# Performance work log

Measured on AMD Instinct MI355X. Metric: run time of the kernel, lower is better.

## Reference

```python
import math
import jax, jax.numpy as jnp
import numpy as np

N_EMBD = 1024
N_HEAD = 16
HEAD_DIM = N_EMBD // N_HEAD


def setup_inputs() -> dict:
    key = jax.random.key(0)
    k1, k2, k3, k4, k5 = jax.random.split(key, 5)
    B, T, C = 1, 4096, N_EMBD
    s = 1.0 / math.sqrt(C)
    return {
        "x": jax.random.normal(k1, (B, T, C), dtype=jnp.float32),
        "w_qkv": jax.random.normal(k2, (C, 3 * C), dtype=jnp.float32) * s,
        "b_qkv": jnp.zeros((3 * C,), dtype=jnp.float32),
        "w_proj": jax.random.normal(k3, (C, C), dtype=jnp.float32) * s,
        "b_proj": jnp.zeros((C,), dtype=jnp.float32),
    }


def reference(x, w_qkv, b_qkv, w_proj, b_proj):
    B, T, C = x.shape
    qkv = x @ w_qkv + b_qkv                       # [B,T,3C]
    q, k, v = jnp.split(qkv, 3, axis=-1)
    # [B,T,C] -> [B,H,T,D]
    def heads(t):
        return t.reshape(B, T, N_HEAD, HEAD_DIM).transpose(0, 2, 1, 3)
    q, k, v = heads(q), heads(k), heads(v)
    scale = 1.0 / math.sqrt(HEAD_DIM)
    attn = jnp.einsum("bhqd,bhkd->bhqk", q, k) * scale
    causal = jnp.tril(jnp.ones((T, T), dtype=bool))
    attn = jnp.where(causal, attn, -jnp.inf)
    attn = jax.nn.softmax(attn, axis=-1)
    out = jnp.einsum("bhqk,bhkd->bhqd", attn, v)   # [B,H,T,D]
    out = out.transpose(0, 2, 1, 3).reshape(B, T, C)
    return out @ w_proj + b_proj
```

## Files before the change

kernel.cpp:

```cpp
#include <hip/hip_runtime.h>
#include <hip/hip_bf16.h>

#define TT 4096
#define CC 1024
#define NHEAD 16
#define DH 64
#define N3C 3072

typedef __attribute__((ext_vector_type(8))) short short8;
typedef __attribute__((ext_vector_type(4))) float floatx4;

#define QSCALE 0.18033688011112042f

__device__ __forceinline__ short f2bf(float f) {
    union { __hip_bfloat16 h; short s; } u;
    u.h = __float2bfloat16(f);
    return u.s;
}

__device__ __forceinline__ void gload_lds16(const void* g, void* l) {
    __builtin_amdgcn_global_load_lds(
        (const __attribute__((address_space(1))) unsigned int*)(unsigned long long)g,
        (__attribute__((address_space(3))) unsigned int*)(unsigned int)(unsigned long long)l,
        16, 0, 0);
}

__device__ __forceinline__ unsigned pk_trunc(float lo, float hi) {
    return __builtin_amdgcn_perm(__float_as_uint(hi), __float_as_uint(lo), 0x07060302u);
}

__device__ __forceinline__ void tr_body(const float* __restrict__ in, short* __restrict__ out,
                                        int K, int N, int bx, int by, int tid, float (*tile)[33]) {
    int nt = bx * 32, kt = by * 32;
    int tx = tid & 31, ty = tid >> 5;
#pragma unroll
    for (int i = 0; i < 32; i += 8)
        tile[ty + i][tx] = in[(size_t)(kt + ty + i) * N + nt + tx];
    __syncthreads();
#pragma unroll
    for (int i = 0; i < 32; i += 8)
        out[(size_t)(nt + ty + i) * K + kt + tx] = f2bf(tile[tx][ty + i]);
}

__global__ void k_prep(const float* __restrict__ x, short* __restrict__ xb,
                       const float* __restrict__ w_qkv, short* __restrict__ wqkvT,
                       const float* __restrict__ w_proj, short* __restrict__ wprojT) {
    __shared__ float tile[32][33];
    int id = blockIdx.x;
    int tid = threadIdx.x;
    if (id < 4096) {
        int i = (id * 256 + tid) * 4;
        float4 v = *(const float4*)&x[i];
        short4 r;
        r.x = f2bf(v.x); r.y = f2bf(v.y); r.z = f2bf(v.z); r.w = f2bf(v.w);
        *(short4*)&xb[i] = r;
    } else if (id < 4096 + 3072) {
        int r = id - 4096;
        tr_body(w_qkv, wqkvT, CC, N3C, r % 96, r / 96, tid, tile);
    } else {
        int r = id - 7168;
        tr_body(w_proj, wprojT, CC, CC, r & 31, r >> 5, tid, tile);
    }
}

__global__ __launch_bounds__(256) void k_gemm_qkv(const short* __restrict__ A,
                                                  const short* __restrict__ Bt,
                                                  const float* __restrict__ bias,
                                                  short* __restrict__ Q,
                                                  short* __restrict__ Kb,
                                                  short* __restrict__ Vtg) {
    const int m0 = blockIdx.y * 128;
    const int n0 = blockIdx.x * 128;
    __shared__ __attribute__((aligned(16))) short As[2][128 * 32];
    __shared__ __attribute__((aligned(16))) short Bs[2][128 * 32];
    const int tid = threadIdx.x;
    const int lane = tid & 63;
    const int w = tid >> 6;
    const int wm = w >> 1, wn = w & 1;
    const int quad = lane >> 4;
    const int l16 = lane & 15;

    const int r0 = tid >> 2, c0 = (tid & 3) * 8;
    const short* pA[2][2]; const short* pB[2][2];
    short* lA[2][2]; short* lB[2][2];
#pragma unroll
    for (int it = 0; it < 2; ++it)
#pragma unroll
        for (int hh = 0; hh < 2; ++hh) {
            pA[it][hh] = A + (size_t)(m0 + it * 64 + r0) * CC + hh * 32 + c0;
            pB[it][hh] = Bt + (size_t)(n0 + it * 64 + r0) * CC + hh * 32 + c0;
            lA[it][hh] = &As[hh][(it * 256 + w * 64) * 8];
            lB[it][hh] = &Bs[hh][(it * 256 + w * 64) * 8];
        }

    floatx4 acc[4][4] = {};
    for (int kb = 0; kb < CC; kb += 64) {
        __syncthreads();
#pragma unroll
        for (int it = 0; it < 2; ++it)
#pragma unroll
            for (int hh = 0; hh < 2; ++hh) {
                gload_lds16(pA[it][hh] + kb, lA[it][hh]);
                gload_lds16(pB[it][hh] + kb, lB[it][hh]);
            }
        __syncthreads();
#pragma unroll
        for (int kk = 0; kk < 2; ++kk) {
            short8 af[4], bf[4];
#pragma unroll
            for (int mi = 0; mi < 4; ++mi)
                af[mi] = *(const short8*)&As[kk][(wm * 64 + mi * 16 + l16) * 32 + quad * 8];
#pragma unroll
            for (int ni = 0; ni < 4; ++ni)
                bf[ni] = *(const short8*)&Bs[kk][(wn * 64 + ni * 16 + l16) * 32 + quad * 8];
#pragma unroll
            for (int mi = 0; mi < 4; ++mi)
#pragma unroll
                for (int ni = 0; ni < 4; ++ni)
                    acc[mi][ni] = __builtin_amdgcn_mfma_f32_16x16x32_bf16(af[mi], bf[ni], acc[mi][ni], 0, 0, 0);
        }
    }
#pragma unroll
    for (int mi = 0; mi < 4; ++mi) {
#pragma unroll
        for (int ni = 0; ni < 4; ++ni) {
            int gm = m0 + wm * 64 + mi * 16 + quad * 4;
            int gn = n0 + wn * 64 + ni * 16 + l16;
            int which = gn >> 10;
            int cc = gn & 1023;
            int h = cc >> 6, d = cc & 63;
            float bv = bias[gn];
            if (which == 0) {
#pragma unroll
                for (int r = 0; r < 4; ++r) {
                    float v = (acc[mi][ni][r] + bv) * QSCALE;
                    Q[((size_t)h * TT + (gm + r)) * DH + d] = f2bf(v);
                }
            } else if (which == 1) {
#pragma unroll
                for (int r = 0; r < 4; ++r) {
                    float v = acc[mi][ni][r] + bv;
                    Kb[((size_t)h * TT + (gm + r)) * DH + d] = f2bf(v);
                }
            } else {
                short4 vv;
                vv.x = f2bf(acc[mi][ni][0] + bv);
                vv.y = f2bf(acc[mi][ni][1] + bv);
                vv.z = f2bf(acc[mi][ni][2] + bv);
                vv.w = f2bf(acc[mi][ni][3] + bv);
                *(short4*)&Vtg[((size_t)h * DH + d) * TT + gm] = vv;
            }
        }
    }
}

__global__ __launch_bounds__(256) void k_attn(const short* __restrict__ Qh,
                                              const short* __restrict__ Kh,
                                              const short* __restrict__ VhT,
                                              short* __restrict__ Ob) {
    const int h = blockIdx.x;
    const int qi = 63 - blockIdx.y;
    const int tid = threadIdx.x, lane = tid & 63, w = tid >> 6;
    const int quad = lane >> 4, l16 = lane & 15;

    __shared__ __attribute__((aligned(16))) short Ps[2][64 * 136];
    __shared__ float wl[4][64];
    __shared__ float lsum[64];

    const short* Qp = Qh + (size_t)h * TT * DH;
    const short* Kp = Kh + (size_t)h * TT * DH;
    const short* Vp = VhT + (size_t)h * DH * TT;

    const int q0 = qi * 64;
    const int nk = (qi >> 1) + 1;

    short8 aq[4][2];
#pragma unroll
    for (int qg = 0; qg < 4; ++qg)
#pragma unroll
        for (int s = 0; s < 2; ++s)
            aq[qg][s] = *(const short8*)&Qp[(size_t)(q0 + qg * 16 + l16) * DH + s * 32 + quad * 8];

    floatx4 accO[4] = {};
    float l_part[4] = {0.f, 0.f, 0.f, 0.f};
    int buf = 0;

    for (int ki = 0; ki < nk; ++ki) {
        const int k0 = ki * 128;
        const bool masked = (ki == nk - 1);

        short8 kf[2][2];
#pragma unroll
        for (int mi = 0; mi < 2; ++mi)
#pragma unroll
            for (int s = 0; s < 2; ++s)
                kf[mi][s] = *(const short8*)&Kp[(size_t)(k0 + w * 32 + mi * 16 + l16) * DH + s * 32 + quad * 8];

        floatx4 accS[2][4] = {};
#pragma unroll
        for (int mi = 0; mi < 2; ++mi)
#pragma unroll
            for (int s = 0; s < 2; ++s)
#pragma unroll
                for (int qg = 0; qg < 4; ++qg)
                    accS[mi][qg] = __builtin_amdgcn_mfma_f32_16x16x32_bf16(kf[mi][s], aq[qg][s], accS[mi][qg], 0, 0, 0);

        short* Pb = &Ps[buf][0];
#pragma unroll
        for (int mi = 0; mi < 2; ++mi) {
            const int kbase = k0 + w * 32 + mi * 16 + quad * 4;
#pragma unroll
            for (int qg = 0; qg < 4; ++qg) {
                float p[4];
#pragma unroll
                for (int r = 0; r < 4; ++r) {
                    float e = __builtin_amdgcn_exp2f(accS[mi][qg][r]);
                    if (masked)
                        e = (kbase + r <= q0 + qg * 16 + l16) ? e : 0.f;
                    p[r] = e;
                    l_part[qg] += e;
                }
                uint2 pk;
                pk.x = pk_trunc(p[0], p[1]);
                pk.y = pk_trunc(p[2], p[3]);
                *(uint2*)&Pb[(qg * 16 + l16) * 136 + w * 32 + mi * 16 + quad * 4] = pk;
            }
        }

        short8 vf[4];
#pragma unroll
        for (int ks = 0; ks < 4; ++ks)
            vf[ks] = *(const short8*)&Vp[(size_t)(w * 16 + l16) * TT + k0 + ks * 32 + quad * 8];

        __syncthreads();

#pragma unroll
        for (int qg = 0; qg < 4; ++qg)
#pragma unroll
            for (int ks = 0; ks < 4; ++ks) {
                short8 ap = *(const short8*)&Pb[(qg * 16 + l16) * 136 + ks * 32 + quad * 8];
                accO[qg] = __builtin_amdgcn_mfma_f32_16x16x32_bf16(ap, vf[ks], accO[qg], 0, 0, 0);
            }
        buf ^= 1;
    }

#pragma unroll
    for (int qg = 0; qg < 4; ++qg) {
        float lr = l_part[qg];
        lr += __shfl_xor(lr, 16, 64);
        lr += __shfl_xor(lr, 32, 64);
        if (lane < 16) wl[w][qg * 16 + lane] = lr;
    }
    __syncthreads();
    if (tid < 64) lsum[tid] = wl[0][tid] + wl[1][tid] + wl[2][tid] + wl[3][tid];
    __syncthreads();

#pragma unroll
    for (int qg = 0; qg < 4; ++qg) {
#pragma unroll
        for (int r = 0; r < 4; ++r) {
            int q = qg * 16 + quad * 4 + r;
            float o = accO[qg][r] / lsum[q];
            Ob[(size_t)(q0 + q) * CC + h * DH + w * 16 + l16] = f2bf(o);
        }
    }
}

__global__ __launch_bounds__(256) void k_gemm_proj(const short* __restrict__ A,
                                                   const short* __restrict__ Bt,
                                                   const float* __restrict__ bias,
                                                   float* __restrict__ out) {
    const int m0 = blockIdx.y * 128;
    const int n0 = blockIdx.x * 128;
    __shared__ __attribute__((aligned(16))) short As[2][128 * 32];
    __shared__ __attribute__((aligned(16))) short Bs[2][128 * 32];
    const int tid = threadIdx.x;
    const int lane = tid & 63;
    const int w = tid >> 6;
    const int wm = w >> 1, wn = w & 1;
    const int quad = lane >> 4;
    const int l16 = lane & 15;

    const int r0 = tid >> 2, c0 = (tid & 3) * 8;
    const short* pA[2][2]; const short* pB[2][2];
    short* lA[2][2]; short* lB[2][2];
#pragma unroll
    for (int it = 0; it < 2; ++it)
#pragma unroll
        for (int hh = 0; hh < 2; ++hh) {
            pA[it][hh] = A + (size_t)(m0 + it * 64 + r0) * CC + hh * 32 + c0;
            pB[it][hh] = Bt + (size_t)(n0 + it * 64 + r0) * CC + hh * 32 + c0;
            lA[it][hh] = &As[hh][(it * 256 + w * 64) * 8];
            lB[it][hh] = &Bs[hh][(it * 256 + w * 64) * 8];
        }

    floatx4 acc[4][4] = {};
    for (int kb = 0; kb < CC; kb += 64) {
        __syncthreads();
#pragma unroll
        for (int it = 0; it < 2; ++it)
#pragma unroll
            for (int hh = 0; hh < 2; ++hh) {
                gload_lds16(pA[it][hh] + kb, lA[it][hh]);
                gload_lds16(pB[it][hh] + kb, lB[it][hh]);
            }
        __syncthreads();
#pragma unroll
        for (int kk = 0; kk < 2; ++kk) {
            short8 af[4], bf[4];
#pragma unroll
            for (int mi = 0; mi < 4; ++mi)
                af[mi] = *(const short8*)&As[kk][(wm * 64 + mi * 16 + l16) * 32 + quad * 8];
#pragma unroll
            for (int ni = 0; ni < 4; ++ni)
                bf[ni] = *(const short8*)&Bs[kk][(wn * 64 + ni * 16 + l16) * 32 + quad * 8];
#pragma unroll
            for (int mi = 0; mi < 4; ++mi)
#pragma unroll
                for (int ni = 0; ni < 4; ++ni)
                    acc[mi][ni] = __builtin_amdgcn_mfma_f32_16x16x32_bf16(af[mi], bf[ni], acc[mi][ni], 0, 0, 0);
        }
    }
#pragma unroll
    for (int mi = 0; mi < 4; ++mi) {
#pragma unroll
        for (int ni = 0; ni < 4; ++ni) {
            int gm = m0 + wm * 64 + mi * 16 + quad * 4;
            int gn = n0 + wn * 64 + ni * 16 + l16;
            float bv = bias[gn];
#pragma unroll
            for (int r = 0; r < 4; ++r)
                out[(size_t)(gm + r) * CC + gn] = acc[mi][ni][r] + bv;
        }
    }
}

extern "C" void kernel_launch(void* const* d_in, const int* in_sizes, int n_in,
                              void* d_out, int out_size, void* d_ws, size_t ws_size,
                              hipStream_t stream) {
    const float* x      = (const float*)d_in[0];
    const float* w_qkv  = (const float*)d_in[1];
    const float* b_qkv  = (const float*)d_in[2];
    const float* w_proj = (const float*)d_in[3];
    const float* b_proj = (const float*)d_in[4];
    float* out = (float*)d_out;
    char* ws = (char*)d_ws;

    short* xb     = (short*)(ws);
    short* wqkvT  = (short*)(ws + 8388608);
    short* wprojT = (short*)(ws + 14680064);
    short* Qh     = (short*)(ws + 16777216);
    short* Kh     = (short*)(ws + 25165824);
    short* VhT    = (short*)(ws + 33554432);
    short* Ob     = (short*)(ws + 41943040);

    k_prep<<<8192, 256, 0, stream>>>(x, xb, w_qkv, wqkvT, w_proj, wprojT);
    k_gemm_qkv<<<dim3(N3C / 128, TT / 128), 256, 0, stream>>>(xb, wqkvT, b_qkv, Qh, Kh, VhT);
    k_attn<<<dim3(NHEAD, 64), 256, 0, stream>>>(Qh, Kh, VhT, Ob);
    k_gemm_proj<<<dim3(CC / 128, TT / 128), 256, 0, stream>>>(Ob, wprojT, b_proj, out);
}
```

Before: 214.9 us.

## Remap attention blocks to balance causal work and raise MFMA wave priority

Changes the attention grid to a 1D launch of 1024 blocks and maps block indices so that heavy (late) query tiles are scheduled first, interleaved with light ones, to balance causal-mask work across CUs. Also raises wave priority around the two MFMA loops with s_setprio. Loop variables are renamed to avoid a clash with the new index variable. The mapping must still cover every head and query tile exactly once, and the setprio effect depends on how waves get scheduled.

```diff
diff --git a/kernel.cpp b/kernel.cpp
--- a/kernel.cpp
+++ b/kernel.cpp
@@ -158,8 +158,16 @@
                                               const short* __restrict__ Kh,
                                               const short* __restrict__ VhT,
                                               short* __restrict__ Ob) {
-    const int h = blockIdx.x;
-    const int qi = 63 - blockIdx.y;
+    const int b = blockIdx.x;
+    const int s = b >> 8;
+    const int c = b & 255;
+    const int p = (s == 0 || s == 3) ? c : c + 256;
+    const int heavy = (s <= 1);
+    const int h = p & 15;
+    const int pr = p >> 4;
+    const int qlin = 2 * (pr & 15) + (pr >> 4);
+    const int qi = heavy ? (63 - qlin) : qlin;
+
     const int tid = threadIdx.x, lane = tid & 63, w = tid >> 6;
     const int quad = lane >> 4, l16 = lane & 15;
 
@@ -178,8 +186,8 @@
 #pragma unroll
     for (int qg = 0; qg < 4; ++qg)
 #pragma unroll
-        for (int s = 0; s < 2; ++s)
-            aq[qg][s] = *(const short8*)&Qp[(size_t)(q0 + qg * 16 + l16) * DH + s * 32 + quad * 8];
+        for (int ss = 0; ss < 2; ++ss)
+            aq[qg][ss] = *(const short8*)&Qp[(size_t)(q0 + qg * 16 + l16) * DH + ss * 32 + quad * 8];
 
     floatx4 accO[4] = {};
     float l_part[4] = {0.f, 0.f, 0.f, 0.f};
@@ -193,17 +201,19 @@
 #pragma unroll
         for (int mi = 0; mi < 2; ++mi)
 #pragma unroll
-            for (int s = 0; s < 2; ++s)
-                kf[mi][s] = *(const short8*)&Kp[(size_t)(k0 + w * 32 + mi * 16 + l16) * DH + s * 32 + quad * 8];
+            for (int ss = 0; ss < 2; ++ss)
+                kf[mi][ss] = *(const short8*)&Kp[(size_t)(k0 + w * 32 + mi * 16 + l16) * DH + ss * 32 + quad * 8];
 
         floatx4 accS[2][4] = {};
+        __builtin_amdgcn_s_setprio(1);
 #pragma unroll
         for (int mi = 0; mi < 2; ++mi)
 #pragma unroll
-            for (int s = 0; s < 2; ++s)
+            for (int ss = 0; ss < 2; ++ss)
 #pragma unroll
                 for (int qg = 0; qg < 4; ++qg)
-                    accS[mi][qg] = __builtin_amdgcn_mfma_f32_16x16x32_bf16(kf[mi][s], aq[qg][s], accS[mi][qg], 0, 0, 0);
+                    accS[mi][qg] = __builtin_amdgcn_mfma_f32_16x16x32_bf16(kf[mi][ss], aq[qg][ss], accS[mi][qg], 0, 0, 0);
+        __builtin_amdgcn_s_setprio(0);
 
         short* Pb = &Ps[buf][0];
 #pragma unroll
@@ -211,18 +221,18 @@
             const int kbase = k0 + w * 32 + mi * 16 + quad * 4;
 #pragma unroll
             for (int qg = 0; qg < 4; ++qg) {
-                float p[4];
+                float pv[4];
 #pragma unroll
                 for (int r = 0; r < 4; ++r) {
                     float e = __builtin_amdgcn_exp2f(accS[mi][qg][r]);
                     if (masked)
                         e = (kbase + r <= q0 + qg * 16 + l16) ? e : 0.f;
-                    p[r] = e;
+                    pv[r] = e;
                     l_part[qg] += e;
                 }
                 uint2 pk;
-                pk.x = pk_trunc(p[0], p[1]);
-                pk.y = pk_trunc(p[2], p[3]);
+                pk.x = pk_trunc(pv[0], pv[1]);
+                pk.y = pk_trunc(pv[2], pv[3]);
                 *(uint2*)&Pb[(qg * 16 + l16) * 136 + w * 32 + mi * 16 + quad * 4] = pk;
             }
         }
@@ -234,6 +244,7 @@
 
         __syncthreads();
 
+        __builtin_amdgcn_s_setprio(1);
 #pragma unroll
         for (int qg = 0; qg < 4; ++qg)
 #pragma unroll
@@ -241,6 +252,7 @@
                 short8 ap = *(const short8*)&Pb[(qg * 16 + l16) * 136 + ks * 32 + quad * 8];
                 accO[qg] = __builtin_amdgcn_mfma_f32_16x16x32_bf16(ap, vf[ks], accO[qg], 0, 0, 0);
             }
+        __builtin_amdgcn_s_setprio(0);
         buf ^= 1;
     }
 
@@ -356,6 +368,6 @@
 
     k_prep<<<8192, 256, 0, stream>>>(x, xb, w_qkv, wqkvT, w_proj, wprojT);
     k_gemm_qkv<<<dim3(N3C / 128, TT / 128), 256, 0, stream>>>(xb, wqkvT, b_qkv, Qh, Kh, VhT);
-    k_attn<<<dim3(NHEAD, 64), 256, 0, stream>>>(Qh, Kh, VhT, Ob);
+    k_attn<<<1024, 256, 0, stream>>>(Qh, Kh, VhT, Ob);
     k_gemm_proj<<<dim3(CC / 128, TT / 128), 256, 0, stream>>>(Ob, wprojT, b_proj, out);
 }
```

New measurement: 230.5 us. 1.07x slower.

## Rewrite attention as single-wave 32x32 MFMA blocks with register-resident P

Applied to the files above, without the earlier changes.

The attention kernel now runs one 64-thread wave per block, covering 32 query rows with 32x32x16 bf16 MFMAs over 32-key tiles. The P tile is repacked in registers with v_permlane32_swap, which removes the LDS staging buffer and the per-tile __syncthreads. Causal work is balanced by pairing long and short query blocks in the launch order. The cost is that each wave loads its own K and V fragments from global memory or L2, with no sharing across waves, and the grid has twice as many smaller blocks.

```diff
diff --git a/kernel.cpp b/kernel.cpp
--- a/kernel.cpp
+++ b/kernel.cpp
@@ -9,6 +9,8 @@
 
 typedef __attribute__((ext_vector_type(8))) short short8;
 typedef __attribute__((ext_vector_type(4))) float floatx4;
+typedef __attribute__((ext_vector_type(16))) float floatx16;
+typedef __attribute__((ext_vector_type(4))) unsigned int uint4v;
 
 #define QSCALE 0.18033688011112042f
 
@@ -154,115 +156,98 @@
     }
 }
 
-__global__ __launch_bounds__(256) void k_attn(const short* __restrict__ Qh,
-                                              const short* __restrict__ Kh,
-                                              const short* __restrict__ VhT,
-                                              short* __restrict__ Ob) {
+__global__ __launch_bounds__(64) void k_attn(const short* __restrict__ Qh,
+                                             const short* __restrict__ Kh,
+                                             const short* __restrict__ VhT,
+                                             short* __restrict__ Ob) {
     const int h = blockIdx.x;
-    const int qi = 63 - blockIdx.y;
-    const int tid = threadIdx.x, lane = tid & 63, w = tid >> 6;
-    const int quad = lane >> 4, l16 = lane & 15;
-
-    __shared__ __attribute__((aligned(16))) short Ps[2][64 * 136];
-    __shared__ float wl[4][64];
-    __shared__ float lsum[64];
+    const int y = blockIdx.y;
+    const int u = (y < 64) ? (127 - 2 * y) : (2 * (y - 64));
+    const int qi = u >> 1, qsub = u & 1;
+    const int qb = qi * 64 + qsub * 32;
+    const int nk = u + 1;
+
+    const int lane = threadIdx.x;
+    const int l31 = lane & 31;
+    const int hi = lane >> 5;
 
     const short* Qp = Qh + (size_t)h * TT * DH;
     const short* Kp = Kh + (size_t)h * TT * DH;
     const short* Vp = VhT + (size_t)h * DH * TT;
 
-    const int q0 = qi * 64;
-    const int nk = (qi >> 1) + 1;
-
-    short8 aq[4][2];
-#pragma unroll
-    for (int qg = 0; qg < 4; ++qg)
-#pragma unroll
-        for (int s = 0; s < 2; ++s)
-            aq[qg][s] = *(const short8*)&Qp[(size_t)(q0 + qg * 16 + l16) * DH + s * 32 + quad * 8];
-
-    floatx4 accO[4] = {};
-    float l_part[4] = {0.f, 0.f, 0.f, 0.f};
-    int buf = 0;
+    short8 bq[4];
+#pragma unroll
+    for (int st = 0; st < 4; ++st)
+        bq[st] = *(const short8*)&Qp[(size_t)(qb + l31) * DH + st * 16 + hi * 8];
+
+    floatx16 accO0 = {}, accO1 = {};
+    float l_acc = 0.f;
 
     for (int ki = 0; ki < nk; ++ki) {
-        const int k0 = ki * 128;
+        const int k0 = ki * 32;
         const bool masked = (ki == nk - 1);
 
-        short8 kf[2][2];
-#pragma unroll
-        for (int mi = 0; mi < 2; ++mi)
-#pragma unroll
-            for (int s = 0; s < 2; ++s)
-                kf[mi][s] = *(const short8*)&Kp[(size_t)(k0 + w * 32 + mi * 16 + l16) * DH + s * 32 + quad * 8];
-
-        floatx4 accS[2][4] = {};
-#pragma unroll
-        for (int mi = 0; mi < 2; ++mi)
-#pragma unroll
-            for (int s = 0; s < 2; ++s)
-#pragma unroll
-                for (int qg = 0; qg < 4; ++qg)
-                    accS[mi][qg] = __builtin_amdgcn_mfma_f32_16x16x32_bf16(kf[mi][s], aq[qg][s], accS[mi][qg], 0, 0, 0);
-
-        short* Pb = &Ps[buf][0];
-#pragma unroll
-        for (int mi = 0; mi < 2; ++mi) {
-            const int kbase = k0 + w * 32 + mi * 16 + quad * 4;
-#pragma unroll
-            for (int qg = 0; qg < 4; ++qg) {
-                float p[4];
-#pragma unroll
-                for (int r = 0; r < 4; ++r) {
-                    float e = __builtin_amdgcn_exp2f(accS[mi][qg][r]);
-                    if (masked)
-                        e = (kbase + r <= q0 + qg * 16 + l16) ? e : 0.f;
-                    p[r] = e;
-                    l_part[qg] += e;
-                }
-                uint2 pk;
-                pk.x = pk_trunc(p[0], p[1]);
-                pk.y = pk_trunc(p[2], p[3]);
-                *(uint2*)&Pb[(qg * 16 + l16) * 136 + w * 32 + mi * 16 + quad * 4] = pk;
+        short8 ak[4];
+#pragma unroll
+        for (int st = 0; st < 4; ++st)
+            ak[st] = *(const short8*)&Kp[(size_t)(k0 + l31) * DH + st * 16 + hi * 8];
+        short8 vf[2][2];
+#pragma unroll
+        for (int db = 0; db < 2; ++db)
+#pragma unroll
+            for (int kst = 0; kst < 2; ++kst)
+                vf[db][kst] = *(const short8*)&Vp[(size_t)(db * 32 + l31) * TT + k0 + kst * 16 + hi * 8];
+
+        floatx16 s = {};
+#pragma unroll
+        for (int st = 0; st < 4; ++st)
+            s = __builtin_amdgcn_mfma_f32_32x32x16_bf16(ak[st], bq[st], s, 0, 0, 0);
+
+        float p[16];
+#pragma unroll
+        for (int r = 0; r < 16; ++r)
+            p[r] = __builtin_amdgcn_exp2f(s[r]);
+        if (masked) {
+            const int qg = qb + l31;
+#pragma unroll
+            for (int r = 0; r < 16; ++r) {
+                int kg = k0 + (r & 3) + 8 * (r >> 2) + 4 * hi;
+                p[r] = (kg <= qg) ? p[r] : 0.f;
             }
         }
-
-        short8 vf[4];
-#pragma unroll
-        for (int ks = 0; ks < 4; ++ks)
-            vf[ks] = *(const short8*)&Vp[(size_t)(w * 16 + l16) * TT + k0 + ks * 32 + quad * 8];
-
-        __syncthreads();
-
-#pragma unroll
-        for (int qg = 0; qg < 4; ++qg)
-#pragma unroll
-            for (int ks = 0; ks < 4; ++ks) {
-                short8 ap = *(const short8*)&Pb[(qg * 16 + l16) * 136 + ks * 32 + quad * 8];
-                accO[qg] = __builtin_amdgcn_mfma_f32_16x16x32_bf16(ap, vf[ks], accO[qg], 0, 0, 0);
-            }
-        buf ^= 1;
-    }
-
-#pragma unroll
-    for (int qg = 0; qg < 4; ++qg) {
-        float lr = l_part[qg];
-        lr += __shfl_xor(lr, 16, 64);
-        lr += __shfl_xor(lr, 32, 64);
-        if (lane < 16) wl[w][qg * 16 + lane] = lr;
-    }
-    __syncthreads();
-    if (tid < 64) lsum[tid] = wl[0][tid] + wl[1][tid] + wl[2][tid] + wl[3][tid];
-    __syncthreads();
-
-#pragma unroll
-    for (int qg = 0; qg < 4; ++qg) {
-#pragma unroll
-        for (int r = 0; r < 4; ++r) {
-            int q = qg * 16 + quad * 4 + r;
-            float o = accO[qg][r] / lsum[q];
-            Ob[(size_t)(q0 + q) * CC + h * DH + w * 16 + l16] = f2bf(o);
-        }
+#pragma unroll
+        for (int r = 0; r < 16; ++r) l_acc += p[r];
+
+        unsigned pa[8];
+        pa[0] = pk_trunc(p[0], p[1]);   pa[1] = pk_trunc(p[2], p[3]);
+        pa[2] = pk_trunc(p[4], p[5]);   pa[3] = pk_trunc(p[6], p[7]);
+        pa[4] = pk_trunc(p[8], p[9]);   pa[5] = pk_trunc(p[10], p[11]);
+        pa[6] = pk_trunc(p[12], p[13]); pa[7] = pk_trunc(p[14], p[15]);
+        asm("v_permlane32_swap_b32 %0, %1" : "+v"(pa[0]), "+v"(pa[2]));
+        asm("v_permlane32_swap_b32 %0, %1" : "+v"(pa[1]), "+v"(pa[3]));
+        asm("v_permlane32_swap_b32 %0, %1" : "+v"(pa[4]), "+v"(pa[6]));
+        asm("v_permlane32_swap_b32 %0, %1" : "+v"(pa[5]), "+v"(pa[7]));
+        uint4v a0v = {pa[0], pa[1], pa[2], pa[3]};
+        uint4v a1v = {pa[4], pa[5], pa[6], pa[7]};
+        short8 A0 = __builtin_bit_cast(short8, a0v);
+        short8 A1 = __builtin_bit_cast(short8, a1v);
+
+        accO0 = __builtin_amdgcn_mfma_f32_32x32x16_bf16(A0, vf[0][0], accO0, 0, 0, 0);
+        accO0 = __builtin_amdgcn_mfma_f32_32x32x16_bf16(A1, vf[0][1], accO0, 0, 0, 0);
+        accO1 = __builtin_amdgcn_mfma_f32_32x32x16_bf16(A0, vf[1][0], accO1, 0, 0, 0);
+        accO1 = __builtin_amdgcn_mfma_f32_32x32x16_bf16(A1, vf[1][1], accO1, 0, 0, 0);
+    }
+
+    l_acc += __shfl_xor(l_acc, 32, 64);
+    float inv = __builtin_amdgcn_rcpf(l_acc);
+
+#pragma unroll
+    for (int r = 0; r < 16; ++r) {
+        int qr = (r & 3) + 8 * (r >> 2) + 4 * hi;
+        float iv = __shfl(inv, qr, 64);
+        int qg = qb + qr;
+        Ob[(size_t)qg * CC + h * DH + l31]      = f2bf(accO0[r] * iv);
+        Ob[(size_t)qg * CC + h * DH + 32 + l31] = f2bf(accO1[r] * iv);
     }
 }
 
@@ -356,6 +341,6 @@
 
     k_prep<<<8192, 256, 0, stream>>>(x, xb, w_qkv, wqkvT, w_proj, wprojT);
     k_gemm_qkv<<<dim3(N3C / 128, TT / 128), 256, 0, stream>>>(xb, wqkvT, b_qkv, Qh, Kh, VhT);
-    k_attn<<<dim3(NHEAD, 64), 256, 0, stream>>>(Qh, Kh, VhT, Ob);
+    k_attn<<<dim3(NHEAD, 128), 64, 0, stream>>>(Qh, Kh, VhT, Ob);
     k_gemm_proj<<<dim3(CC / 128, TT / 128), 256, 0, stream>>>(Ob, wprojT, b_proj, out);
 }
```

Result: slower. 278.3 us (+29.5%).
